# Performance work log

Measured on AMD Instinct MI355X. Metric: run time of the kernel, lower is better.

The kernel has to match this reference:

```python
import jax, jax.numpy as jnp
import numpy as np

B, C, H, W = 64, 3, 256, 256
K = 2  # multi_n_num
EPS_NORM = 1e-8
EPS_DEN = 1e-7
SCALE = 0.01


def setup_inputs() -> dict:
    key = jax.random.key(0)
    ka, kp, kn, kj = jax.random.split(key, 4)
    a = jax.random.normal(ka, (B, C, H, W), dtype=jnp.float32)
    p = jax.random.normal(kp, (B, C, H, W), dtype=jnp.float32)
    n = jax.random.normal(kn, (B, C, H, W), dtype=jnp.float32)
    # sample_with_j(B, 2, i) -> [i, random j != i]
    ar = jnp.arange(B, dtype=jnp.int64)
    off = jax.random.randint(kj, (B,), 1, B)  # offset in [1, B) guarantees j != i
    neg_idx = jnp.stack([ar, (ar + off) % B], axis=1).astype(jnp.int64)  # [B, K]
    return {"a": a, "p": p, "n": n, "neg_idx": neg_idx}


def _fft_norm(x):
    # torch.fft.fft2 over last two dims -> complex, same rank as x
    f = jnp.fft.fft2(x, axes=(-2, -1))  # [B, C, H, W] complex64
    # torch.norm(f, p=2, dim=1, keepdim=True) on complex = sqrt(sum |f|^2 over C)
    nrm = jnp.sqrt(jnp.sum(jnp.abs(f) ** 2, axis=1, keepdims=True))
    return f / (nrm + EPS_NORM) * SCALE


def reference(a, p, n, neg_idx):
    af = _fft_norm(a)
    pf = _fft_norm(p)
    nf = _fft_norm(n)
    # L1Loss on complex tensors = mean |diff| (complex magnitude)
    d_ap = jnp.mean(jnp.abs(af - pf), axis=(1, 2, 3))  # [B]
    n_sel = nf[neg_idx]  # [B, K, C, H, W]
    d_an = jnp.mean(jnp.abs(af[:, None] - n_sel), axis=(2, 3, 4))  # [B, K]
    contrastive = jnp.sum(d_ap[:, None] / (d_an + EPS_DEN))
    return contrastive / (K * B)
```

## Files before the change

kernel.cpp:

```cpp
#include <hip/hip_runtime.h>
#include <hip/hip_fp16.h>

#define B_ 64
#define SW_ 132
#define SIMG_ (256 * SW_)
#define TIMG_ (3 * SIMG_)
#define TELEMS_ ((size_t)B_ * TIMG_)
#define SST_ 257

__device__ __forceinline__ float2 cmul(float2 a, float2 b) {
  return make_float2(a.x * b.x - a.y * b.y, a.x * b.y + a.y * b.x);
}
__device__ __forceinline__ unsigned f2u(float2 v) {
  __half2 h = __float22half2_rn(v);
  return __builtin_bit_cast(unsigned, h);
}
__device__ __forceinline__ float2 u2f(unsigned u) {
  return __half22float2(__builtin_bit_cast(__half2, u));
}

__device__ __forceinline__ void bfly4(float2 x[4], float2 ta, float2 tb, float2 tc, bool tw) {
  float2 a = make_float2(x[0].x + x[2].x, x[0].y + x[2].y);
  float2 b = make_float2(x[0].x - x[2].x, x[0].y - x[2].y);
  float2 c = make_float2(x[1].x + x[3].x, x[1].y + x[3].y);
  float2 d = make_float2(x[1].x - x[3].x, x[1].y - x[3].y);
  float2 y1 = make_float2(b.x + d.y, b.y - d.x);
  float2 y2 = make_float2(a.x - c.x, a.y - c.y);
  float2 y3 = make_float2(b.x - d.y, b.y + d.x);
  x[0] = make_float2(a.x + c.x, a.y + c.y);
  if (tw) { y1 = cmul(y1, ta); y2 = cmul(y2, tb); y3 = cmul(y3, tc); }
  x[1] = y1; x[2] = y2; x[3] = y3;
}

__device__ __forceinline__ void xbit(unsigned& A, unsigned& B, int bit, int r) {
  bool hi = (r >> bit) & 1;
  int send = hi ? (int)A : (int)B;
  int got = __shfl_xor(send, 1 << bit, 64);
  if (hi) A = (unsigned)got; else B = (unsigned)got;
}
__device__ __forceinline__ void xdigit2(unsigned uA[4], unsigned uB[4], int bit, int r) {
  xbit(uA[0], uA[1], bit, r);
  xbit(uA[2], uA[3], bit, r);
  xbit(uB[0], uB[1], bit, r);
  xbit(uB[2], uB[3], bit, r);
  xbit(uA[0], uA[2], bit + 1, r);
  xbit(uA[1], uA[3], bit + 1, r);
  xbit(uB[0], uB[2], bit + 1, r);
  xbit(uB[1], uB[3], bit + 1, r);
}
__device__ __forceinline__ void xdigit(unsigned u[4], int bit, int r) {
  xbit(u[0], u[1], bit, r);
  xbit(u[2], u[3], bit, r);
  xbit(u[0], u[2], bit + 1, r);
  xbit(u[1], u[3], bit + 1, r);
}

__device__ __forceinline__ void fft256_reg2(float2 xA[4], unsigned uA[4],
                                            float2 xB[4], unsigned uB[4],
                                            int r, const float2 tw[9]) {
  bfly4(xA, tw[0], tw[1], tw[2], true);
  bfly4(xB, tw[0], tw[1], tw[2], true);
#pragma unroll
  for (int s = 0; s < 4; ++s) { uA[s] = f2u(xA[s]); uB[s] = f2u(xB[s]); }
  xdigit2(uA, uB, 4, r);
#pragma unroll
  for (int s = 0; s < 4; ++s) { xA[s] = u2f(uA[s]); xB[s] = u2f(uB[s]); }
  bfly4(xA, tw[3], tw[4], tw[5], true);
  bfly4(xB, tw[3], tw[4], tw[5], true);
#pragma unroll
  for (int s = 0; s < 4; ++s) { uA[s] = f2u(xA[s]); uB[s] = f2u(xB[s]); }
  xdigit2(uA, uB, 2, r);
#pragma unroll
  for (int s = 0; s < 4; ++s) { xA[s] = u2f(uA[s]); xB[s] = u2f(uB[s]); }
  bfly4(xA, tw[6], tw[7], tw[8], true);
  bfly4(xB, tw[6], tw[7], tw[8], true);
#pragma unroll
  for (int s = 0; s < 4; ++s) { uA[s] = f2u(xA[s]); uB[s] = f2u(xB[s]); }
  xdigit2(uA, uB, 0, r);
#pragma unroll
  for (int s = 0; s < 4; ++s) { xA[s] = u2f(uA[s]); xB[s] = u2f(uB[s]); }
  bfly4(xA, tw[0], tw[0], tw[0], false);
  bfly4(xB, tw[0], tw[0], tw[0], false);
#pragma unroll
  for (int s = 0; s < 4; ++s) { uA[s] = f2u(xA[s]); uB[s] = f2u(xB[s]); }
}

__device__ __forceinline__ void fft256_reg(float2 x[4], unsigned u[4], int r,
                                           const float2 tw[9]) {
  bfly4(x, tw[0], tw[1], tw[2], true);
#pragma unroll
  for (int s = 0; s < 4; ++s) u[s] = f2u(x[s]);
  xdigit(u, 4, r);
#pragma unroll
  for (int s = 0; s < 4; ++s) x[s] = u2f(u[s]);
  bfly4(x, tw[3], tw[4], tw[5], true);
#pragma unroll
  for (int s = 0; s < 4; ++s) u[s] = f2u(x[s]);
  xdigit(u, 2, r);
#pragma unroll
  for (int s = 0; s < 4; ++s) x[s] = u2f(u[s]);
  bfly4(x, tw[6], tw[7], tw[8], true);
#pragma unroll
  for (int s = 0; s < 4; ++s) u[s] = f2u(x[s]);
  xdigit(u, 0, r);
#pragma unroll
  for (int s = 0; s < 4; ++s) x[s] = u2f(u[s]);
  bfly4(x, tw[0], tw[0], tw[0], false);
#pragma unroll
  for (int s = 0; s < 4; ++s) u[s] = f2u(x[s]);
}

__global__ __launch_bounds__(1024, 4) void fft2_fused(const float* __restrict__ a,
                                                      const float* __restrict__ p,
                                                      const float* __restrict__ n,
                                                      unsigned* __restrict__ outbase) {
  __shared__ unsigned S[129 * SST_];

  int tid = threadIdx.x;
  int wv = tid >> 6;
  int r = tid & 63;
  int tensor = blockIdx.x / 192;
  int plane = blockIdx.x % 192;
  const float* in = (tensor == 0 ? a : (tensor == 1 ? p : n)) + (size_t)plane * 65536;
  unsigned* outp = outbase + (size_t)tensor * TELEMS_ + (size_t)plane * SIMG_;

  float2 tw[9];
  {
    float s, c;
    __sincosf(-6.283185307179586f * (float)r / 256.0f, &s, &c);
    tw[0] = make_float2(c, s); tw[1] = cmul(tw[0], tw[0]); tw[2] = cmul(tw[1], tw[0]);
    __sincosf(-6.283185307179586f * (float)(r & 15) / 64.0f, &s, &c);
    tw[3] = make_float2(c, s); tw[4] = cmul(tw[3], tw[3]); tw[5] = cmul(tw[4], tw[3]);
    __sincosf(-6.283185307179586f * (float)(r & 3) / 16.0f, &s, &c);
    tw[6] = make_float2(c, s); tw[7] = cmul(tw[6], tw[6]); tw[8] = cmul(tw[7], tw[6]);
  }
  int m = ((r & 3) << 4) | (((r >> 2) & 3) << 2) | (r >> 4);
  int mp = (64 - m) & 63;
  int rp = ((mp >> 4) & 3) | (((mp >> 2) & 3) << 2) | ((mp & 3) << 4);

  for (int it = 0; it < 4; ++it) {
    int qA = it * 16 + wv;
    int qB = qA + 64;
    const float* rA = in + (size_t)(2 * qA) * 256;
    const float* rB = in + (size_t)(2 * qB) * 256;
    float2 xA[4], xB[4]; unsigned uA[4], uB[4];
#pragma unroll
    for (int j = 0; j < 4; ++j) {
      xA[j] = make_float2(rA[r + 64 * j], rA[256 + r + 64 * j]);
      xB[j] = make_float2(rB[r + 64 * j], rB[256 + r + 64 * j]);
    }
    fft256_reg2(xA, uA, xB, uB, r, tw);
    unsigned mirA[4], mirB[4];
#pragma unroll
    for (int t = 0; t < 4; ++t) {
      mirA[t] = (unsigned)__shfl((int)uA[t], rp, 64);
      mirB[t] = (unsigned)__shfl((int)uB[t], rp, 64);
    }
#pragma unroll
    for (int s = 0; s < 2; ++s) {
      int k = 64 * s + m;
      int sp = (m == 0) ? ((4 - s) & 3) : (3 - s);
      float2 ZkA = u2f(uA[s]), ZmA = u2f(mirA[sp]);
      float2 ZkB = u2f(uB[s]), ZmB = u2f(mirB[sp]);
      float2 Aa = make_float2(0.5f * (ZkA.x + ZmA.x), 0.5f * (ZkA.y - ZmA.y));
      float2 Ab = make_float2(0.5f * (ZkA.y + ZmA.y), 0.5f * (ZmA.x - ZkA.x));
      float2 Ba = make_float2(0.5f * (ZkB.x + ZmB.x), 0.5f * (ZkB.y - ZmB.y));
      float2 Bb = make_float2(0.5f * (ZkB.y + ZmB.y), 0.5f * (ZmB.x - ZkB.x));
      S[k * SST_ + 2 * qA]     = f2u(Aa);
      S[k * SST_ + 2 * qA + 1] = f2u(Ab);
      S[k * SST_ + 2 * qB]     = f2u(Ba);
      S[k * SST_ + 2 * qB + 1] = f2u(Bb);
    }
    if (r == 0) {
      float2 ZA = u2f(uA[2]), ZB = u2f(uB[2]);
      S[128 * SST_ + 2 * qA]     = f2u(make_float2(ZA.x, 0.0f));
      S[128 * SST_ + 2 * qA + 1] = f2u(make_float2(ZA.y, 0.0f));
      S[128 * SST_ + 2 * qB]     = f2u(make_float2(ZB.x, 0.0f));
      S[128 * SST_ + 2 * qB + 1] = f2u(make_float2(ZB.y, 0.0f));
    }
  }

  __syncthreads();

  for (int it = 0; it < 4; ++it) {
    int cA = it * 16 + wv;
    int cB = cA + 64;
    unsigned* rowA = S + cA * SST_;
    unsigned* rowB = S + cB * SST_;
    float2 xA[4], xB[4]; unsigned uA[4], uB[4];
#pragma unroll
    for (int j = 0; j < 4; ++j) {
      xA[j] = u2f(rowA[r + 64 * j]);
      xB[j] = u2f(rowB[r + 64 * j]);
    }
    fft256_reg2(xA, uA, xB, uB, r, tw);
    *(uint4*)(outp + (size_t)cA * 256 + 4 * r) = make_uint4(uA[0], uA[1], uA[2], uA[3]);
    *(uint4*)(outp + (size_t)cB * 256 + 4 * r) = make_uint4(uB[0], uB[1], uB[2], uB[3]);
  }
  if (wv == 0) {
    unsigned* srow = S + 128 * SST_;
    float2 x[4]; unsigned u[4];
#pragma unroll
    for (int j = 0; j < 4; ++j) x[j] = u2f(srow[r + 64 * j]);
    fft256_reg(x, u, r, tw);
    *(uint4*)(outp + (size_t)128 * 256 + 4 * r) = make_uint4(u[0], u[1], u[2], u[3]);
  }
  if (wv >= 13) {
    int c = 129 + (wv - 13);
    *(uint4*)(outp + (size_t)c * 256 + 4 * r) = make_uint4(0, 0, 0, 0);
  }
}

__device__ __forceinline__ float cab2(float2 v) { return v.x * v.x + v.y * v.y; }

__global__ __launch_bounds__(256) void dist_kernel(const unsigned* __restrict__ af,
                                                   const unsigned* __restrict__ pf,
                                                   const unsigned* __restrict__ nf,
                                                   const int* __restrict__ neg,
                                                   float* __restrict__ acc) {
  int b = blockIdx.y;
  int j = (neg[1] == 0) ? (int)((const long long*)neg)[b * 2 + 1] : neg[b * 2 + 1];
  size_t ab = (size_t)b * TIMG_;
  size_t jb = (size_t)j * TIMG_;
  int t4 = blockIdx.x * 256 + threadIdx.x;
  int flat0 = t4 * 4;
  int k2 = flat0 >> 8;
  float w = (k2 == 0 || k2 >= 128) ? 1.0f : 2.0f;

  unsigned A[3][4], P[3][4], N[3][4], M[3][4];
#pragma unroll
  for (int ch = 0; ch < 3; ++ch) {
    uint4 t;
    t = *(const uint4*)(af + ab + ch * SIMG_ + flat0); A[ch][0]=t.x; A[ch][1]=t.y; A[ch][2]=t.z; A[ch][3]=t.w;
    t = *(const uint4*)(pf + ab + ch * SIMG_ + flat0); P[ch][0]=t.x; P[ch][1]=t.y; P[ch][2]=t.z; P[ch][3]=t.w;
    t = *(const uint4*)(nf + ab + ch * SIMG_ + flat0); N[ch][0]=t.x; N[ch][1]=t.y; N[ch][2]=t.z; N[ch][3]=t.w;
    t = *(const uint4*)(nf + jb + ch * SIMG_ + flat0); M[ch][0]=t.x; M[ch][1]=t.y; M[ch][2]=t.z; M[ch][3]=t.w;
  }
  float s_ap = 0.0f, s_a0 = 0.0f, s_a1 = 0.0f;
#pragma unroll
  for (int e = 0; e < 4; ++e) {
    float2 a0 = u2f(A[0][e]), a1 = u2f(A[1][e]), a2 = u2f(A[2][e]);
    float2 p0 = u2f(P[0][e]), p1 = u2f(P[1][e]), p2 = u2f(P[2][e]);
    float2 n0 = u2f(N[0][e]), n1 = u2f(N[1][e]), n2 = u2f(N[2][e]);
    float2 m0 = u2f(M[0][e]), m1 = u2f(M[1][e]), m2 = u2f(M[2][e]);
    float sa = 0.01f / (sqrtf(cab2(a0) + cab2(a1) + cab2(a2)) + 1e-8f);
    float sp = 0.01f / (sqrtf(cab2(p0) + cab2(p1) + cab2(p2)) + 1e-8f);
    float sn = 0.01f / (sqrtf(cab2(n0) + cab2(n1) + cab2(n2)) + 1e-8f);
    float sm = 0.01f / (sqrtf(cab2(m0) + cab2(m1) + cab2(m2)) + 1e-8f);
    float dx, dy;
    dx = a0.x * sa - p0.x * sp; dy = a0.y * sa - p0.y * sp; s_ap += sqrtf(dx * dx + dy * dy);
    dx = a1.x * sa - p1.x * sp; dy = a1.y * sa - p1.y * sp; s_ap += sqrtf(dx * dx + dy * dy);
    dx = a2.x * sa - p2.x * sp; dy = a2.y * sa - p2.y * sp; s_ap += sqrtf(dx * dx + dy * dy);
    dx = a0.x * sa - n0.x * sn; dy = a0.y * sa - n0.y * sn; s_a0 += sqrtf(dx * dx + dy * dy);
    dx = a1.x * sa - n1.x * sn; dy = a1.y * sa - n1.y * sn; s_a0 += sqrtf(dx * dx + dy * dy);
    dx = a2.x * sa - n2.x * sn; dy = a2.y * sa - n2.y * sn; s_a0 += sqrtf(dx * dx + dy * dy);
    dx = a0.x * sa - m0.x * sm; dy = a0.y * sa - m0.y * sm; s_a1 += sqrtf(dx * dx + dy * dy);
    dx = a1.x * sa - m1.x * sm; dy = a1.y * sa - m1.y * sm; s_a1 += sqrtf(dx * dx + dy * dy);
    dx = a2.x * sa - m2.x * sm; dy = a2.y * sa - m2.y * sm; s_a1 += sqrtf(dx * dx + dy * dy);
  }
  s_ap *= w; s_a0 *= w; s_a1 *= w;
#pragma unroll
  for (int off = 32; off > 0; off >>= 1) {
    s_ap += __shfl_down(s_ap, off);
    s_a0 += __shfl_down(s_a0, off);
    s_a1 += __shfl_down(s_a1, off);
  }
  __shared__ float red[3][4];
  int lane = threadIdx.x & 63, wid = threadIdx.x >> 6;
  if (lane == 0) { red[0][wid] = s_ap; red[1][wid] = s_a0; red[2][wid] = s_a1; }
  __syncthreads();
  if (threadIdx.x == 0) {
    atomicAdd(&acc[b * 3 + 0], red[0][0] + red[0][1] + red[0][2] + red[0][3]);
    atomicAdd(&acc[b * 3 + 1], red[1][0] + red[1][1] + red[1][2] + red[1][3]);
    atomicAdd(&acc[b * 3 + 2], red[2][0] + red[2][1] + red[2][2] + red[2][3]);
  }
}

__global__ void zero_acc(float* acc) { acc[threadIdx.x] = 0.0f; }

__global__ void final_kernel(const float* __restrict__ acc, float* __restrict__ out) {
  int b = threadIdx.x;
  const float inv = 1.0f / 196608.0f;
  float dap = acc[b * 3 + 0] * inv;
  float da0 = acc[b * 3 + 1] * inv;
  float da1 = acc[b * 3 + 2] * inv;
  float term = dap / (da0 + 1e-7f) + dap / (da1 + 1e-7f);
#pragma unroll
  for (int off = 32; off > 0; off >>= 1) term += __shfl_down(term, off);
  if (b == 0) out[0] = term * (1.0f / 128.0f);
}

extern "C" void kernel_launch(void* const* d_in, const int* in_sizes, int n_in,
                              void* d_out, int out_size, void* d_ws, size_t ws_size,
                              hipStream_t stream) {
  const float* a = (const float*)d_in[0];
  const float* p = (const float*)d_in[1];
  const float* n = (const float*)d_in[2];
  const int* neg = (const int*)d_in[3];
  float* out = (float*)d_out;

  unsigned* base = (unsigned*)d_ws;
  float* acc = (float*)(base + 3 * TELEMS_);

  zero_acc<<<1, 192, 0, stream>>>(acc);
  fft2_fused<<<576, 1024, 0, stream>>>(a, p, n, base);
  dist_kernel<<<dim3(33, 64), 256, 0, stream>>>(base, base + TELEMS_,
                                                base + 2 * TELEMS_, neg, acc);
  final_kernel<<<1, 64, 0, stream>>>(acc, out);
}
```

Measured before the change: 246.2 us.

## Replace shuffle exchanges with permlane/DPP/swizzle and batch four FFTs per wave

Replaces the generic __shfl_xor lane exchanges in the register FFT with cheaper cross-lane primitives: v_permlane16/32_swap for the high bits, DPP quad permutes for bits 0-1, and ds_swizzle for bits 2-3. The row and column FFT loops now process four independent FFTs per wave per iteration instead of two, which gives more instruction-level parallelism. The real-to-complex mirror step also skips one unneeded shuffle. The aim is to cut the cost of LDS-backed bpermute shuffles in the FFT stages, at the price of higher register pressure under launch_bounds(1024,4) and reliance on gfx950-specific instructions.

After: 245.9 us. Within noise of the previous version (-0.1%).

```diff
diff --git a/kernel.cpp b/kernel.cpp
--- a/kernel.cpp
+++ b/kernel.cpp
@@ -32,82 +32,88 @@
   x[1] = y1; x[2] = y2; x[3] = y3;
 }
 
-__device__ __forceinline__ void xbit(unsigned& A, unsigned& B, int bit, int r) {
-  bool hi = (r >> bit) & 1;
+__device__ __forceinline__ void swap16(unsigned& A, unsigned& B) {
+  asm("v_permlane16_swap_b32 %0, %1" : "+v"(A), "+v"(B));
+}
+__device__ __forceinline__ void swap32(unsigned& A, unsigned& B) {
+  asm("v_permlane32_swap_b32 %0, %1" : "+v"(A), "+v"(B));
+}
+
+template <int BIT>
+__device__ __forceinline__ void xsel(unsigned& A, unsigned& B, int r) {
+  bool hi = (r >> BIT) & 1;
   int send = hi ? (int)A : (int)B;
-  int got = __shfl_xor(send, 1 << bit, 64);
+  int got;
+  if constexpr (BIT == 0)
+    got = __builtin_amdgcn_update_dpp(0, send, 0xB1, 0xF, 0xF, false);
+  else if constexpr (BIT == 1)
+    got = __builtin_amdgcn_update_dpp(0, send, 0x4E, 0xF, 0xF, false);
+  else if constexpr (BIT == 2)
+    got = __builtin_amdgcn_ds_swizzle(send, 0x101F);
+  else
+    got = __builtin_amdgcn_ds_swizzle(send, 0x201F);
   if (hi) A = (unsigned)got; else B = (unsigned)got;
 }
-__device__ __forceinline__ void xdigit2(unsigned uA[4], unsigned uB[4], int bit, int r) {
-  xbit(uA[0], uA[1], bit, r);
-  xbit(uA[2], uA[3], bit, r);
-  xbit(uB[0], uB[1], bit, r);
-  xbit(uB[2], uB[3], bit, r);
-  xbit(uA[0], uA[2], bit + 1, r);
-  xbit(uA[1], uA[3], bit + 1, r);
-  xbit(uB[0], uB[2], bit + 1, r);
-  xbit(uB[1], uB[3], bit + 1, r);
-}
-__device__ __forceinline__ void xdigit(unsigned u[4], int bit, int r) {
-  xbit(u[0], u[1], bit, r);
-  xbit(u[2], u[3], bit, r);
-  xbit(u[0], u[2], bit + 1, r);
-  xbit(u[1], u[3], bit + 1, r);
-}
-
-__device__ __forceinline__ void fft256_reg2(float2 xA[4], unsigned uA[4],
-                                            float2 xB[4], unsigned uB[4],
-                                            int r, const float2 tw[9]) {
-  bfly4(xA, tw[0], tw[1], tw[2], true);
-  bfly4(xB, tw[0], tw[1], tw[2], true);
-#pragma unroll
-  for (int s = 0; s < 4; ++s) { uA[s] = f2u(xA[s]); uB[s] = f2u(xB[s]); }
-  xdigit2(uA, uB, 4, r);
-#pragma unroll
-  for (int s = 0; s < 4; ++s) { xA[s] = u2f(uA[s]); xB[s] = u2f(uB[s]); }
-  bfly4(xA, tw[3], tw[4], tw[5], true);
-  bfly4(xB, tw[3], tw[4], tw[5], true);
-#pragma unroll
-  for (int s = 0; s < 4; ++s) { uA[s] = f2u(xA[s]); uB[s] = f2u(xB[s]); }
-  xdigit2(uA, uB, 2, r);
-#pragma unroll
-  for (int s = 0; s < 4; ++s) { xA[s] = u2f(uA[s]); xB[s] = u2f(uB[s]); }
-  bfly4(xA, tw[6], tw[7], tw[8], true);
-  bfly4(xB, tw[6], tw[7], tw[8], true);
-#pragma unroll
-  for (int s = 0; s < 4; ++s) { uA[s] = f2u(xA[s]); uB[s] = f2u(xB[s]); }
-  xdigit2(uA, uB, 0, r);
-#pragma unroll
-  for (int s = 0; s < 4; ++s) { xA[s] = u2f(uA[s]); xB[s] = u2f(uB[s]); }
-  bfly4(xA, tw[0], tw[0], tw[0], false);
-  bfly4(xB, tw[0], tw[0], tw[0], false);
-#pragma unroll
-  for (int s = 0; s < 4; ++s) { uA[s] = f2u(xA[s]); uB[s] = f2u(xB[s]); }
-}
-
-__device__ __forceinline__ void fft256_reg(float2 x[4], unsigned u[4], int r,
-                                           const float2 tw[9]) {
-  bfly4(x, tw[0], tw[1], tw[2], true);
-#pragma unroll
-  for (int s = 0; s < 4; ++s) u[s] = f2u(x[s]);
-  xdigit(u, 4, r);
-#pragma unroll
-  for (int s = 0; s < 4; ++s) x[s] = u2f(u[s]);
-  bfly4(x, tw[3], tw[4], tw[5], true);
-#pragma unroll
-  for (int s = 0; s < 4; ++s) u[s] = f2u(x[s]);
-  xdigit(u, 2, r);
-#pragma unroll
-  for (int s = 0; s < 4; ++s) x[s] = u2f(u[s]);
-  bfly4(x, tw[6], tw[7], tw[8], true);
-#pragma unroll
-  for (int s = 0; s < 4; ++s) u[s] = f2u(x[s]);
-  xdigit(u, 0, r);
-#pragma unroll
-  for (int s = 0; s < 4; ++s) x[s] = u2f(u[s]);
-  bfly4(x, tw[0], tw[0], tw[0], false);
-#pragma unroll
-  for (int s = 0; s < 4; ++s) u[s] = f2u(x[s]);
+
+__device__ __forceinline__ void xdig45(unsigned u[4]) {
+  swap16(u[0], u[1]);
+  swap16(u[2], u[3]);
+  swap32(u[0], u[2]);
+  swap32(u[1], u[3]);
+}
+template <int BIT>
+__device__ __forceinline__ void xdig(unsigned u[4], int r) {
+  xsel<BIT>(u[0], u[1], r);
+  xsel<BIT>(u[2], u[3], r);
+  xsel<BIT + 1>(u[0], u[2], r);
+  xsel<BIT + 1>(u[1], u[3], r);
+}
+
+template <int NF>
+__device__ __forceinline__ void fft256(float2 (&x)[NF][4], unsigned (&u)[NF][4],
+                                       int r, const float2 tw[9]) {
+#pragma unroll
+  for (int f = 0; f < NF; ++f) bfly4(x[f], tw[0], tw[1], tw[2], true);
+#pragma unroll
+  for (int f = 0; f < NF; ++f)
+#pragma unroll
+    for (int s = 0; s < 4; ++s) u[f][s] = f2u(x[f][s]);
+#pragma unroll
+  for (int f = 0; f < NF; ++f) xdig45(u[f]);
+#pragma unroll
+  for (int f = 0; f < NF; ++f)
+#pragma unroll
+    for (int s = 0; s < 4; ++s) x[f][s] = u2f(u[f][s]);
+#pragma unroll
+  for (int f = 0; f < NF; ++f) bfly4(x[f], tw[3], tw[4], tw[5], true);
+#pragma unroll
+  for (int f = 0; f < NF; ++f)
+#pragma unroll
+    for (int s = 0; s < 4; ++s) u[f][s] = f2u(x[f][s]);
+#pragma unroll
+  for (int f = 0; f < NF; ++f) xdig<2>(u[f], r);
+#pragma unroll
+  for (int f = 0; f < NF; ++f)
+#pragma unroll
+    for (int s = 0; s < 4; ++s) x[f][s] = u2f(u[f][s]);
+#pragma unroll
+  for (int f = 0; f < NF; ++f) bfly4(x[f], tw[6], tw[7], tw[8], true);
+#pragma unroll
+  for (int f = 0; f < NF; ++f)
+#pragma unroll
+    for (int s = 0; s < 4; ++s) u[f][s] = f2u(x[f][s]);
+#pragma unroll
+  for (int f = 0; f < NF; ++f) xdig<0>(u[f], r);
+#pragma unroll
+  for (int f = 0; f < NF; ++f)
+#pragma unroll
+    for (int s = 0; s < 4; ++s) x[f][s] = u2f(u[f][s]);
+#pragma unroll
+  for (int f = 0; f < NF; ++f) bfly4(x[f], tw[0], tw[0], tw[0], false);
+#pragma unroll
+  for (int f = 0; f < NF; ++f)
+#pragma unroll
+    for (int s = 0; s < 4; ++s) u[f][s] = f2u(x[f][s]);
 }
 
 __global__ __launch_bounds__(1024, 4) void fft2_fused(const float* __restrict__ a,
@@ -138,72 +144,69 @@
   int mp = (64 - m) & 63;
   int rp = ((mp >> 4) & 3) | (((mp >> 2) & 3) << 2) | ((mp & 3) << 4);
 
-  for (int it = 0; it < 4; ++it) {
-    int qA = it * 16 + wv;
-    int qB = qA + 64;
-    const float* rA = in + (size_t)(2 * qA) * 256;
-    const float* rB = in + (size_t)(2 * qB) * 256;
-    float2 xA[4], xB[4]; unsigned uA[4], uB[4];
-#pragma unroll
-    for (int j = 0; j < 4; ++j) {
-      xA[j] = make_float2(rA[r + 64 * j], rA[256 + r + 64 * j]);
-      xB[j] = make_float2(rB[r + 64 * j], rB[256 + r + 64 * j]);
+  for (int it = 0; it < 2; ++it) {
+    float2 x[4][4]; unsigned u[4][4];
+#pragma unroll
+    for (int f = 0; f < 4; ++f) {
+      int q = it * 64 + wv + 16 * f;
+      const float* rw = in + (size_t)(2 * q) * 256;
+#pragma unroll
+      for (int j = 0; j < 4; ++j)
+        x[f][j] = make_float2(rw[r + 64 * j], rw[256 + r + 64 * j]);
     }
-    fft256_reg2(xA, uA, xB, uB, r, tw);
-    unsigned mirA[4], mirB[4];
-#pragma unroll
-    for (int t = 0; t < 4; ++t) {
-      mirA[t] = (unsigned)__shfl((int)uA[t], rp, 64);
-      mirB[t] = (unsigned)__shfl((int)uB[t], rp, 64);
+    fft256<4>(x, u, r, tw);
+#pragma unroll
+    for (int f = 0; f < 4; ++f) {
+      int q = it * 64 + wv + 16 * f;
+      unsigned m0 = (unsigned)__shfl((int)u[f][0], rp, 64);
+      unsigned m2 = (unsigned)__shfl((int)u[f][2], rp, 64);
+      unsigned m3 = (unsigned)__shfl((int)u[f][3], rp, 64);
+      float2 Zk0 = u2f(u[f][0]);
+      float2 Zk1 = u2f(u[f][1]);
+      float2 Zm0 = u2f((m == 0) ? m0 : m3);
+      float2 Zm1 = u2f((m == 0) ? m3 : m2);
+      float2 Aa = make_float2(0.5f * (Zk0.x + Zm0.x), 0.5f * (Zk0.y - Zm0.y));
+      float2 Ab = make_float2(0.5f * (Zk0.y + Zm0.y), 0.5f * (Zm0.x - Zk0.x));
+      float2 Ba = make_float2(0.5f * (Zk1.x + Zm1.x), 0.5f * (Zk1.y - Zm1.y));
+      float2 Bb = make_float2(0.5f * (Zk1.y + Zm1.y), 0.5f * (Zm1.x - Zk1.x));
+      S[m * SST_ + 2 * q]          = f2u(Aa);
+      S[m * SST_ + 2 * q + 1]      = f2u(Ab);
+      S[(64 + m) * SST_ + 2 * q]     = f2u(Ba);
+      S[(64 + m) * SST_ + 2 * q + 1] = f2u(Bb);
+      if (r == 0) {
+        float2 Z = u2f(u[f][2]);
+        S[128 * SST_ + 2 * q]     = f2u(make_float2(Z.x, 0.0f));
+        S[128 * SST_ + 2 * q + 1] = f2u(make_float2(Z.y, 0.0f));
+      }
     }
-#pragma unroll
-    for (int s = 0; s < 2; ++s) {
-      int k = 64 * s + m;
-      int sp = (m == 0) ? ((4 - s) & 3) : (3 - s);
-      float2 ZkA = u2f(uA[s]), ZmA = u2f(mirA[sp]);
-      float2 ZkB = u2f(uB[s]), ZmB = u2f(mirB[sp]);
-      float2 Aa = make_float2(0.5f * (ZkA.x + ZmA.x), 0.5f * (ZkA.y - ZmA.y));
-      float2 Ab = make_float2(0.5f * (ZkA.y + ZmA.y), 0.5f * (ZmA.x - ZkA.x));
-      float2 Ba = make_float2(0.5f * (ZkB.x + ZmB.x), 0.5f * (ZkB.y - ZmB.y));
-      float2 Bb = make_float2(0.5f * (ZkB.y + ZmB.y), 0.5f * (ZmB.x - ZkB.x));
-      S[k * SST_ + 2 * qA]     = f2u(Aa);
-      S[k * SST_ + 2 * qA + 1] = f2u(Ab);
-      S[k * SST_ + 2 * qB]     = f2u(Ba);
-      S[k * SST_ + 2 * qB + 1] = f2u(Bb);
+  }
+
+  __syncthreads();
+
+  for (int it = 0; it < 2; ++it) {
+    float2 x[4][4]; unsigned u[4][4];
+#pragma unroll
+    for (int f = 0; f < 4; ++f) {
+      const unsigned* row = S + (size_t)(it * 64 + wv + 16 * f) * SST_;
+#pragma unroll
+      for (int j = 0; j < 4; ++j) x[f][j] = u2f(row[r + 64 * j]);
     }
-    if (r == 0) {
-      float2 ZA = u2f(uA[2]), ZB = u2f(uB[2]);
-      S[128 * SST_ + 2 * qA]     = f2u(make_float2(ZA.x, 0.0f));
-      S[128 * SST_ + 2 * qA + 1] = f2u(make_float2(ZA.y, 0.0f));
-      S[128 * SST_ + 2 * qB]     = f2u(make_float2(ZB.x, 0.0f));
-      S[128 * SST_ + 2 * qB + 1] = f2u(make_float2(ZB.y, 0.0f));
+    fft256<4>(x, u, r, tw);
+#pragma unroll
+    for (int f = 0; f < 4; ++f) {
+      int c = it * 64 + wv + 16 * f;
+      *(uint4*)(outp + (size_t)c * 256 + 4 * r) =
+          make_uint4(u[f][0], u[f][1], u[f][2], u[f][3]);
     }
   }
-
-  __syncthreads();
-
-  for (int it = 0; it < 4; ++it) {
-    int cA = it * 16 + wv;
-    int cB = cA + 64;
-    unsigned* rowA = S + cA * SST_;
-    unsigned* rowB = S + cB * SST_;
-    float2 xA[4], xB[4]; unsigned uA[4], uB[4];
-#pragma unroll
-    for (int j = 0; j < 4; ++j) {
-      xA[j] = u2f(rowA[r + 64 * j]);
-      xB[j] = u2f(rowB[r + 64 * j]);
-    }
-    fft256_reg2(xA, uA, xB, uB, r, tw);
-    *(uint4*)(outp + (size_t)cA * 256 + 4 * r) = make_uint4(uA[0], uA[1], uA[2], uA[3]);
-    *(uint4*)(outp + (size_t)cB * 256 + 4 * r) = make_uint4(uB[0], uB[1], uB[2], uB[3]);
-  }
   if (wv == 0) {
-    unsigned* srow = S + 128 * SST_;
-    float2 x[4]; unsigned u[4];
-#pragma unroll
-    for (int j = 0; j < 4; ++j) x[j] = u2f(srow[r + 64 * j]);
-    fft256_reg(x, u, r, tw);
-    *(uint4*)(outp + (size_t)128 * 256 + 4 * r) = make_uint4(u[0], u[1], u[2], u[3]);
+    float2 x1[1][4]; unsigned u1[1][4];
+    const unsigned* srow = S + 128 * SST_;
+#pragma unroll
+    for (int j = 0; j < 4; ++j) x1[0][j] = u2f(srow[r + 64 * j]);
+    fft256<1>(x1, u1, r, tw);
+    *(uint4*)(outp + (size_t)128 * 256 + 4 * r) =
+        make_uint4(u1[0][0], u1[0][1], u1[0][2], u1[0][3]);
   }
   if (wv >= 13) {
     int c = 129 + (wv - 13);
```
